# Optimization experiments

Measured on AMD Instinct MI355X. Metric: run time of the kernel, lower is better.

The kernel has to match this reference:

```python
import jax, jax.numpy as jnp
import numpy as np

DIM = 384
HEADS = 12
WS = (7, 7, 7)
N = WS[0] * WS[1] * WS[2]  # 343
NW = 64   # number of windows (mask dim)
B_ = 64   # num_windows * batch
CPB_HIDDEN = 512


def _make_buffers():
    # relative coords table: (1, 2Wd-1, 2Wh-1, 2Ww-1, 3), log-spaced per Swin-V2
    axes = [np.arange(-(w - 1), w, dtype=np.float32) / (w - 1) for w in WS]
    g = np.stack(np.meshgrid(*axes, indexing='ij'), axis=-1)[None]  # (1,13,13,13,3)
    g = g * 8.0
    table = np.sign(g) * np.log2(np.abs(g) + 1.0) / np.log2(8.0)
    # relative position index: (N, N) int
    coords = np.stack(np.meshgrid(*[np.arange(w) for w in WS], indexing='ij'))  # (3,Wd,Wh,Ww)
    cf = coords.reshape(3, -1)
    rel = (cf[:, :, None] - cf[:, None, :]).transpose(1, 2, 0).astype(np.int64)  # (N,N,3)
    rel[..., 0] += WS[0] - 1
    rel[..., 1] += WS[1] - 1
    rel[..., 2] += WS[2] - 1
    rel[..., 0] *= (2 * WS[1] - 1) * (2 * WS[2] - 1)
    rel[..., 1] *= 2 * WS[2] - 1
    idx = rel.sum(-1)
    return jnp.asarray(table, dtype=jnp.float32), jnp.asarray(idx, dtype=jnp.int32)


def setup_inputs() -> dict:
    key = jax.random.key(0)
    ks = jax.random.split(key, 10)
    table, idx = _make_buffers()
    return {
        'x': jax.random.normal(ks[0], (B_, N, DIM), dtype=jnp.float32),
        'mask': jax.random.normal(ks[1], (NW, N, N), dtype=jnp.float32),
        'qkv_w': jax.random.normal(ks[2], (3 * DIM, DIM), dtype=jnp.float32) * 0.02,
        'q_bias': jax.random.normal(ks[3], (DIM,), dtype=jnp.float32) * 0.02,
        'v_bias': jax.random.normal(ks[4], (DIM,), dtype=jnp.float32) * 0.02,
        'logit_scale': jnp.log(10.0 * jnp.ones((HEADS, 1, 1), dtype=jnp.float32)),
        'cpb_w1': jax.random.normal(ks[5], (CPB_HIDDEN, 3), dtype=jnp.float32) * 0.02,
        'cpb_b1': jax.random.normal(ks[6], (CPB_HIDDEN,), dtype=jnp.float32) * 0.02,
        'cpb_w2': jax.random.normal(ks[7], (HEADS, CPB_HIDDEN), dtype=jnp.float32) * 0.02,
        'proj_w': jax.random.normal(ks[8], (DIM, DIM), dtype=jnp.float32) * 0.02,
        'proj_b': jax.random.normal(ks[9], (DIM,), dtype=jnp.float32) * 0.02,
        'rel_table': table,
        'rel_index': idx,
    }


def reference(x, mask, qkv_w, q_bias, v_bias, logit_scale, cpb_w1, cpb_b1,
              cpb_w2, proj_w, proj_b, rel_table, rel_index):
    Bw, n, C = x.shape
    H = logit_scale.shape[0]
    hd = C // H
    qkv_bias = jnp.concatenate([q_bias, jnp.zeros_like(v_bias), v_bias])
    qkv = x @ qkv_w.T + qkv_bias                      # (Bw, n, 3C)
    qkv = qkv.reshape(Bw, n, 3, H, hd).transpose(2, 0, 3, 1, 4)
    q, k, v = qkv[0], qkv[1], qkv[2]                  # (Bw, H, n, hd)
    qn = q / jnp.clip(jnp.linalg.norm(q, axis=-1, keepdims=True), 1e-12)
    kn = k / jnp.clip(jnp.linalg.norm(k, axis=-1, keepdims=True), 1e-12)
    attn = jnp.einsum('bhnd,bhmd->bhnm', qn, kn)
    scale = jnp.exp(jnp.minimum(logit_scale, jnp.log(100.0)))  # clamp max log(1/0.01)
    attn = attn * scale
    # CPB MLP bias: (1,13,13,13,3) -> (table_size, H), gathered to (H, n, n)
    hidden = jax.nn.relu(rel_table @ cpb_w1.T + cpb_b1)
    bias_table = (hidden @ cpb_w2.T).reshape(-1, H)
    bias = bias_table[rel_index.reshape(-1)].reshape(n, n, H).transpose(2, 0, 1)
    bias = 16.0 * jax.nn.sigmoid(bias)
    attn = attn + bias[None]
    nW = mask.shape[0]
    attn = attn.reshape(Bw // nW, nW, H, n, n) + mask[None, :, None]
    attn = attn.reshape(Bw, H, n, n)
    attn = jax.nn.softmax(attn, axis=-1)
    out = jnp.einsum('bhnm,bhmd->bnhd', attn, v).reshape(Bw, n, C)
    out = out @ proj_w.T + proj_b
    return out
```

## Files before the change

### kernel.cpp

```cpp
#include <hip/hip_runtime.h>
#include <hip/hip_bf16.h>
#include <stdint.h>


typedef __attribute__((ext_vector_type(4))) float f32x4;
typedef __attribute__((ext_vector_type(8))) short short8;

#define DIM   384
#define HEADS 12
#define NTOK  343
#define NPAD  352
#define BW    64
#define MROWS (BW*NTOK)
#define MPAD  22016
#define NN    (NTOK*NTOK)
#define BPAD  352
#define LOG2E 1.44269504089f
#define SMAX  48.0f

__device__ __forceinline__ unsigned short f2bf(float f) {
  unsigned u = __float_as_uint(f);
  u += 0x7FFF + ((u >> 16) & 1);
  return (unsigned short)(u >> 16);
}

__device__ __forceinline__ unsigned pk2bf(float lo, float hi) {
  return (__float_as_uint(hi) & 0xFFFF0000u) | (__float_as_uint(lo) >> 16);
}

__device__ __forceinline__ void gload_lds16(const void* g, void* l) {
  __builtin_amdgcn_global_load_lds(
      (const __attribute__((address_space(1))) void*)g,
      (__attribute__((address_space(3))) void*)l, 16, 0, 0);
}

__global__ __launch_bounds__(256) void cvt_bf16(const float* __restrict__ in,
                                                unsigned short* __restrict__ out,
                                                long nvalid, long ntotal) {
  long i = ((long)blockIdx.x * 256 + threadIdx.x) * 8;
  if (i >= ntotal) return;
  short8 o;
  if (i < nvalid) {
    const float4* p = (const float4*)(in + i);
    float4 a = p[0], b = p[1];
    o[0] = (short)f2bf(a.x); o[1] = (short)f2bf(a.y);
    o[2] = (short)f2bf(a.z); o[3] = (short)f2bf(a.w);
    o[4] = (short)f2bf(b.x); o[5] = (short)f2bf(b.y);
    o[6] = (short)f2bf(b.z); o[7] = (short)f2bf(b.w);
  } else {
    o = (short8)0;
  }
  *(short8*)(out + i) = o;
}

__global__ __launch_bounds__(64) void cpb_tab(const float* __restrict__ tbl,
                                              const float* __restrict__ w1,
                                              const float* __restrict__ b1,
                                              const float* __restrict__ w2,
                                              float* __restrict__ btab) {
  const int r = blockIdx.x, lane = threadIdx.x;
  const float t0 = tbl[r*3], t1 = tbl[r*3+1], t2 = tbl[r*3+2];
  float acc[12];
#pragma unroll
  for (int hh = 0; hh < 12; ++hh) acc[hh] = 0.f;
  for (int u = 0; u < 8; ++u) {
    const int j = lane * 8 + u;
    const float hd = fmaxf(w1[j*3]*t0 + w1[j*3+1]*t1 + w1[j*3+2]*t2 + b1[j], 0.f);
#pragma unroll
    for (int hh = 0; hh < 12; ++hh) acc[hh] += hd * w2[hh*512 + j];
  }
#pragma unroll
  for (int hh = 0; hh < 12; ++hh) {
    float v = acc[hh];
    for (int msk = 1; msk < 64; msk <<= 1) v += __shfl_xor(v, msk);
    if (lane == 0) btab[r*12 + hh] = v;
  }
}

__global__ __launch_bounds__(256) void bias_gather(const float* __restrict__ btab,
                                                   const int* __restrict__ ridx,
                                                   float* __restrict__ bfull) {
  const int blk = blockIdx.x;
  const int hh = blk / NTOK, i = blk % NTOK;
  for (int j = threadIdx.x; j < BPAD; j += 256) {
    float o = -1e9f;
    if (j < NTOK) {
      const int idx = ridx[i*NTOK + j];
      const float v = btab[idx*12 + hh];
      o = LOG2E * 16.f / (1.f + __expf(-v)) - SMAX;
    }
    bfull[(size_t)blk*BPAD + j] = o;
  }
}

template<int MODE>
__global__ __launch_bounds__(256, 2) void gemm_k(
    const unsigned short* __restrict__ A, const unsigned short* __restrict__ B,
    unsigned short* __restrict__ o_qn, unsigned short* __restrict__ o_kn,
    unsigned short* __restrict__ o_vT,
    const float* __restrict__ q_bias, const float* __restrict__ v_bias,
    const float* __restrict__ lsc,
    float* __restrict__ o_out, const float* __restrict__ proj_b) {
  __shared__ alignas(16) uint8_t lds[32768];
  const int tid = threadIdx.x, wave = tid >> 6, lane = tid & 63;
  const int row0 = blockIdx.x * 128, col0 = blockIdx.y * 128;
  const int wm = wave & 1, wn = wave >> 1;
  const int l15 = lane & 15, lq = lane >> 4;
  f32x4 acc[4][4];
#pragma unroll
  for (int i = 0; i < 4; ++i)
#pragma unroll
    for (int j = 0; j < 4; ++j) acc[i][j] = (f32x4)0.f;

  const int stg_row = wave * 8 + (lane >> 3);
  const int srcblk = (lane & 7) ^ (lane >> 3);

  for (int kt = 0; kt < 6; ++kt) {
    const int k0 = kt * 64;
#pragma unroll
    for (int c = 0; c < 4; ++c) {
      const int row = c * 32 + stg_row;
      gload_lds16(A + (size_t)(row0 + row) * DIM + k0 + srcblk * 8,
                  lds + c * 4096 + wave * 1024);
      gload_lds16(B + (size_t)(col0 + row) * DIM + k0 + srcblk * 8,
                  lds + 16384 + c * 4096 + wave * 1024);
    }
    __syncthreads();
#pragma unroll
    for (int s = 0; s < 2; ++s) {
      short8 af[4], bfr[4];
#pragma unroll
      for (int i = 0; i < 4; ++i) {
        const int r = wm * 64 + i * 16 + l15;
        af[i] = *(const short8*)(lds + r * 128 + (((s * 4) | lq) ^ (r & 7)) * 16);
        const int cc = wn * 64 + i * 16 + l15;
        bfr[i] = *(const short8*)(lds + 16384 + cc * 128 + (((s * 4) | lq) ^ (cc & 7)) * 16);
      }
#pragma unroll
      for (int i = 0; i < 4; ++i)
#pragma unroll
        for (int j = 0; j < 4; ++j)
          acc[i][j] = __builtin_amdgcn_mfma_f32_16x16x32_bf16(af[i], bfr[j], acc[i][j], 0, 0, 0);
    }
    __syncthreads();
  }

  if (MODE == 0) {
#pragma unroll
    for (int i = 0; i < 4; ++i) {
      const int gr0 = row0 + wm * 64 + i * 16 + lq * 4;
#pragma unroll
      for (int p = 0; p < 2; ++p) {
        f32x4 c0 = acc[i][2 * p], c1 = acc[i][2 * p + 1];
        const int gcb = col0 + wn * 64 + p * 32;
        const int which = gcb / DIM, rem = gcb % DIM, hh = rem / 32;
        float b0 = 0.f, b1 = 0.f;
        if (which == 0) { b0 = q_bias[rem + l15]; b1 = q_bias[rem + l15 + 16]; }
        else if (which == 2) { b0 = v_bias[rem + l15]; b1 = v_bias[rem + l15 + 16]; }
#pragma unroll
        for (int r = 0; r < 4; ++r) { c0[r] += b0; c1[r] += b1; }
        float mult[4] = {1.f, 1.f, 1.f, 1.f};
        if (which < 2) {
          f32x4 ss;
#pragma unroll
          for (int r = 0; r < 4; ++r) ss[r] = c0[r] * c0[r] + c1[r] * c1[r];
#pragma unroll
          for (int msk = 1; msk < 16; msk <<= 1) {
#pragma unroll
            for (int r = 0; r < 4; ++r) ss[r] += __shfl_xor(ss[r], msk);
          }
          float sc = 1.f;
          if (which == 0)
            sc = __expf(fminf(lsc[hh], 4.6051701860f)) * LOG2E;
#pragma unroll
          for (int r = 0; r < 4; ++r) mult[r] = sc / fmaxf(sqrtf(ss[r]), 1e-12f);
        }
#pragma unroll
        for (int r = 0; r < 4; ++r) {
          const int gr = gr0 + r;
          if (gr >= MROWS) continue;
          const int b = gr / NTOK, nt = gr % NTOK;
          const unsigned short v0 = f2bf(c0[r] * mult[r]);
          const unsigned short v1 = f2bf(c1[r] * mult[r]);
          if (which == 0) {
            const size_t base = ((size_t)(b * HEADS + hh) * NTOK + nt) * 32 + l15;
            o_qn[base] = v0; o_qn[base + 16] = v1;
          } else if (which == 1) {
            const size_t base = ((size_t)(b * HEADS + hh) * NTOK + nt) * 32 + l15;
            o_kn[base] = v0; o_kn[base + 16] = v1;
          } else {
            const size_t base = ((size_t)(b * HEADS + hh) * 32 + l15) * NPAD + nt;
            o_vT[base] = v0; o_vT[base + (size_t)16 * NPAD] = v1;
          }
        }
      }
    }
  } else {
#pragma unroll
    for (int i = 0; i < 4; ++i) {
      const int gr0 = row0 + wm * 64 + i * 16 + lq * 4;
#pragma unroll
      for (int j = 0; j < 4; ++j) {
        const int gc = col0 + wn * 64 + j * 16 + l15;
        const float pb = proj_b[gc];
#pragma unroll
        for (int r = 0; r < 4; ++r) {
          const int gr = gr0 + r;
          if (gr < MROWS) o_out[(size_t)gr * DIM + gc] = acc[i][j][r] + pb;
        }
      }
    }
  }
}

__global__ __launch_bounds__(256, 3) void attn_k(
    const unsigned short* __restrict__ qn, const unsigned short* __restrict__ kn,
    const unsigned short* __restrict__ vT, const float* __restrict__ bfull,
    const float* __restrict__ mask, unsigned short* __restrict__ out1) {
  __shared__ alignas(16) uint8_t lds[38400];
  const int g = blockIdx.x;
  const int b = (g & 7) * 8 + (g >> 3) / HEADS;
  const int hh = (g >> 3) % HEADS;
  const int bh = b * HEADS + hh;
  const int tid = threadIdx.x;

  for (int r = tid; r < NPAD; r += 256) {
    uint4* dst = (uint4*)(lds + r * 80);
    if (r < NTOK) {
      const uint4* src = (const uint4*)(kn + ((size_t)bh * NTOK + r) * 32);
      dst[0] = src[0]; dst[1] = src[1]; dst[2] = src[2]; dst[3] = src[3];
    } else {
      uint4 z = make_uint4(0, 0, 0, 0);
      dst[0] = z; dst[1] = z; dst[2] = z; dst[3] = z;
    }
  }
  __syncthreads();

  const int wave = tid >> 6, lane = tid & 63;
  const int l15 = lane & 15, lq = lane >> 4;
  uint8_t* pb0 = lds + 28160 + wave * 2560;
  uint8_t* pb1 = pb0 + 1280;

  const unsigned short* vrow0 = vT + ((size_t)bh * 32 + 2 * l15) * NPAD;
  const unsigned short* vrow1 = vT + ((size_t)bh * 32 + 2 * l15 + 1) * NPAD;

  for (int t = wave; t < 22; t += 4) {
    const int q0 = t * 16;
    const int qc = min(q0 + l15, NTOK - 1);
    const short8 aq = *(const short8*)(qn + ((size_t)bh * NTOK + qc) * 32 + lq * 8);
    const float* brow = bfull + ((size_t)hh * NTOK + qc) * BPAD;
    const float* mrow = mask + (size_t)b * NN + (size_t)qc * NTOK;

    f32x4 o0 = (f32x4)0.f, o1 = (f32x4)0.f;
    float l_run = 0.f;

    f32x4 pbA[2], pbB[2];
    float pmA[2][4], pmB[2][4];
    short8 kf0[2], kf1[2], vf0[2], vf1[2];

    pbA[0] = *(const f32x4*)(brow + lq * 4);
    pbB[0] = *(const f32x4*)(brow + 16 + lq * 4);
    pbA[1] = *(const f32x4*)(brow + 32 + lq * 4);
    pbB[1] = *(const f32x4*)(brow + 48 + lq * 4);
#pragma unroll
    for (int r = 0; r < 4; ++r) {
      pmA[0][r] = mrow[lq * 4 + r];
      pmB[0][r] = mrow[16 + lq * 4 + r];
      pmA[1][r] = mrow[32 + lq * 4 + r];
      pmB[1][r] = mrow[48 + lq * 4 + r];
    }
    kf0[0] = *(const short8*)(lds + l15 * 80 + lq * 16);
    kf1[0] = *(const short8*)(lds + (16 + l15) * 80 + lq * 16);
    vf0[0] = *(const short8*)(vrow0 + lq * 8);
    vf1[0] = *(const short8*)(vrow1 + lq * 8);

#pragma unroll
    for (int c = 0; c <= 10; ++c) {
      const int cur = c & 1, nxt = cur ^ 1;
      const f32x4 cBA = pbA[cur], cBB = pbB[cur];
      float cMA[4], cMB[4];
#pragma unroll
      for (int r = 0; r < 4; ++r) { cMA[r] = pmA[cur][r]; cMB[r] = pmB[cur][r]; }
      const short8 vA = vf0[nxt], vB = vf1[nxt];
      if (c <= 8) {
        const int k2 = (c + 2) * 32;
        pbA[cur] = *(const f32x4*)(brow + k2 + lq * 4);
        pbB[cur] = *(const f32x4*)(brow + k2 + 16 + lq * 4);
#pragma unroll
        for (int r = 0; r < 4; ++r) {
          pmA[cur][r] = mrow[k2 + lq * 4 + r];
          const int kk = k2 + 16 + lq * 4 + r;
          pmB[cur][r] = mrow[(c == 8 && kk >= NTOK) ? 0 : kk];
        }
      }
      if (c <= 9) {
        const int k1 = (c + 1) * 32;
        vf0[nxt] = *(const short8*)(vrow0 + k1 + lq * 8);
        vf1[nxt] = *(const short8*)(vrow1 + k1 + lq * 8);
        kf0[nxt] = *(const short8*)(lds + (k1 + l15) * 80 + lq * 16);
        kf1[nxt] = *(const short8*)(lds + (k1 + 16 + l15) * 80 + lq * 16);
      }
      short8 pf;
      if (c > 0) pf = *(const short8*)((nxt ? pb1 : pb0) + l15 * 80 + lq * 16);
      f32x4 s0 = __builtin_amdgcn_mfma_f32_16x16x32_bf16(kf0[cur], aq, (f32x4)0.f, 0, 0, 0);
      f32x4 s1 = __builtin_amdgcn_mfma_f32_16x16x32_bf16(kf1[cur], aq, (f32x4)0.f, 0, 0, 0);
      float p0[4], p1[4], ps = 0.f;
#pragma unroll
      for (int r = 0; r < 4; ++r) {
        p0[r] = exp2f(s0[r] + fmaf(cMA[r], LOG2E, cBA[r]));
        p1[r] = exp2f(s1[r] + fmaf(cMB[r], LOG2E, cBB[r]));
        ps += p0[r] + p1[r];
      }
      l_run += ps;
      uint8_t* pw = (cur ? pb1 : pb0) + l15 * 80;
      *(uint2*)(pw + lq * 8)      = make_uint2(pk2bf(p0[0], p0[1]), pk2bf(p0[2], p0[3]));
      *(uint2*)(pw + 32 + lq * 8) = make_uint2(pk2bf(p1[0], p1[1]), pk2bf(p1[2], p1[3]));
      if (c > 0) {
        o0 = __builtin_amdgcn_mfma_f32_16x16x32_bf16(pf, vA, o0, 0, 0, 0);
        o1 = __builtin_amdgcn_mfma_f32_16x16x32_bf16(pf, vB, o1, 0, 0, 0);
      }
    }
    {
      const short8 pf = *(const short8*)(pb0 + l15 * 80 + lq * 16);
      o0 = __builtin_amdgcn_mfma_f32_16x16x32_bf16(pf, vf0[0], o0, 0, 0, 0);
      o1 = __builtin_amdgcn_mfma_f32_16x16x32_bf16(pf, vf1[0], o1, 0, 0, 0);
    }
    l_run += __shfl_xor(l_run, 16);
    l_run += __shfl_xor(l_run, 32);
    const float invl = 1.f / l_run;
    float ir[4];
#pragma unroll
    for (int r = 0; r < 4; ++r) ir[r] = __shfl(invl, lq * 4 + r);
#pragma unroll
    for (int r = 0; r < 4; ++r) {
      const int q = q0 + lq * 4 + r;
      if (q < NTOK) {
        const size_t base = ((size_t)b * NTOK + q) * DIM + hh * 32 + 2 * l15;
        *(unsigned*)(out1 + base) =
            (((unsigned)f2bf(o1[r] * ir[r])) << 16) | f2bf(o0[r] * ir[r]);
      }
    }
  }
}

extern "C" void kernel_launch(void* const* d_in, const int* in_sizes, int n_in,
                              void* d_out, int out_size, void* d_ws, size_t ws_size,
                              hipStream_t stream) {
  const float* x      = (const float*)d_in[0];
  const float* mask   = (const float*)d_in[1];
  const float* qkv_w  = (const float*)d_in[2];
  const float* q_bias = (const float*)d_in[3];
  const float* v_bias = (const float*)d_in[4];
  const float* lsc    = (const float*)d_in[5];
  const float* cpb_w1 = (const float*)d_in[6];
  const float* cpb_b1 = (const float*)d_in[7];
  const float* cpb_w2 = (const float*)d_in[8];
  const float* proj_w = (const float*)d_in[9];
  const float* proj_b = (const float*)d_in[10];
  const float* rtab   = (const float*)d_in[11];
  const int*   ridx   = (const int*)d_in[12];
  float* out = (float*)d_out;
  uint8_t* ws = (uint8_t*)d_ws;

  size_t o = 0;
  auto alloc = [&](size_t bytes) { size_t r = o; o += (bytes + 255) & ~(size_t)255; return r; };
  const size_t off_xb  = alloc((size_t)MPAD * DIM * 2);
  const size_t off_qwb = alloc((size_t)1152 * DIM * 2);
  const size_t off_pwb = alloc((size_t)DIM * DIM * 2);
  const size_t off_qnb = alloc((size_t)BW * HEADS * NTOK * 32 * 2);
  const size_t off_knb = alloc((size_t)BW * HEADS * NTOK * 32 * 2);
  const size_t off_vTb = alloc((size_t)BW * HEADS * 32 * NPAD * 2);
  const size_t off_btab  = alloc((size_t)2197 * 12 * 4);
  const size_t off_bfull = alloc((size_t)HEADS * NTOK * BPAD * 4);
  (void)in_sizes; (void)n_in; (void)out_size;

  if (ws_size < o) {
    hipMemsetAsync(d_out, 0, (size_t)out_size * 4, stream);
    return;
  }

  unsigned short* xb  = (unsigned short*)(ws + off_xb);
  unsigned short* o1b = xb;
  unsigned short* qwb = (unsigned short*)(ws + off_qwb);
  unsigned short* pwb = (unsigned short*)(ws + off_pwb);
  unsigned short* qnb = (unsigned short*)(ws + off_qnb);
  unsigned short* knb = (unsigned short*)(ws + off_knb);
  unsigned short* vTb = (unsigned short*)(ws + off_vTb);
  float* btab  = (float*)(ws + off_btab);
  float* bfull = (float*)(ws + off_bfull);

  cvt_bf16<<<(long)MPAD * DIM / 8 / 256, 256, 0, stream>>>(x, xb, (long)MROWS * DIM, (long)MPAD * DIM);
  cvt_bf16<<<1152 * DIM / 8 / 256, 256, 0, stream>>>(qkv_w, qwb, 1152L * DIM, 1152L * DIM);
  cvt_bf16<<<DIM * DIM / 8 / 256, 256, 0, stream>>>(proj_w, pwb, (long)DIM * DIM, (long)DIM * DIM);
  cpb_tab<<<2197, 64, 0, stream>>>(rtab, cpb_w1, cpb_b1, cpb_w2, btab);
  bias_gather<<<HEADS * NTOK, 256, 0, stream>>>(btab, ridx, bfull);
  gemm_k<0><<<dim3(MPAD / 128, 1152 / 128), 256, 0, stream>>>(
      xb, qwb, qnb, knb, vTb, q_bias, v_bias, lsc, nullptr, nullptr);
  attn_k<<<BW * HEADS, 256, 0, stream>>>(qnb, knb, vTb, bfull, mask, o1b);
  gemm_k<1><<<dim3(MPAD / 128, DIM / 128), 256, 0, stream>>>(
      o1b, pwb, nullptr, nullptr, nullptr, nullptr, nullptr, nullptr, out, proj_b);
}
```

Measured before the change: 322.8 us.

## Split attention into one-wave blocks per query tile and pre-pad scaled mask

The attention kernel now launches one 64-thread block per (window, head, 16-query tile) instead of one 256-thread block per (window, head) that staged all of K in LDS. K fragments are read straight from global memory, which drops the LDS fill and the block barrier and raises the block count for better occupancy and load balance. A new mask_pad kernel copies the mask into a 352-wide padded layout pre-multiplied by log2(e), so the attention loop can use vector loads without bounds checks and one fewer FMA. In exchange, K is re-read from global or L2 by each of the 22 query tiles, and the extra pass writes about 31 MB of padded mask and reads it back.

```diff
diff --git a/kernel.cpp b/kernel.cpp
--- a/kernel.cpp
+++ b/kernel.cpp
@@ -91,6 +91,15 @@
     }
     bfull[(size_t)blk*BPAD + j] = o;
   }
+}
+
+__global__ __launch_bounds__(128) void mask_pad(const float* __restrict__ mask,
+                                                float* __restrict__ maskp) {
+  const int row = blockIdx.x;
+  const float* src = mask + (size_t)row * NTOK;
+  float* dst = maskp + (size_t)row * BPAD;
+  for (int j = threadIdx.x; j < BPAD; j += 128)
+    dst[j] = (j < NTOK) ? src[j] * LOG2E : 0.f;
 }
 
 template<int MODE>
@@ -213,132 +222,110 @@
   }
 }
 
-__global__ __launch_bounds__(256, 3) void attn_k(
+__global__ __launch_bounds__(64) void attn_k(
     const unsigned short* __restrict__ qn, const unsigned short* __restrict__ kn,
     const unsigned short* __restrict__ vT, const float* __restrict__ bfull,
-    const float* __restrict__ mask, unsigned short* __restrict__ out1) {
-  __shared__ alignas(16) uint8_t lds[38400];
+    const float* __restrict__ maskp, unsigned short* __restrict__ out1) {
+  __shared__ alignas(16) uint8_t lds[2560];
   const int g = blockIdx.x;
-  const int b = (g & 7) * 8 + (g >> 3) / HEADS;
-  const int hh = (g >> 3) % HEADS;
+  const int hi = g >> 3;
+  const int b = (g & 7) * 8 + hi / 264;
+  const int rem = hi % 264;
+  const int hh = rem / 22, t = rem % 22;
   const int bh = b * HEADS + hh;
-  const int tid = threadIdx.x;
-
-  for (int r = tid; r < NPAD; r += 256) {
-    uint4* dst = (uint4*)(lds + r * 80);
-    if (r < NTOK) {
-      const uint4* src = (const uint4*)(kn + ((size_t)bh * NTOK + r) * 32);
-      dst[0] = src[0]; dst[1] = src[1]; dst[2] = src[2]; dst[3] = src[3];
-    } else {
-      uint4 z = make_uint4(0, 0, 0, 0);
-      dst[0] = z; dst[1] = z; dst[2] = z; dst[3] = z;
-    }
-  }
-  __syncthreads();
-
-  const int wave = tid >> 6, lane = tid & 63;
+  const int lane = threadIdx.x;
   const int l15 = lane & 15, lq = lane >> 4;
-  uint8_t* pb0 = lds + 28160 + wave * 2560;
-  uint8_t* pb1 = pb0 + 1280;
+  uint8_t* pb0 = lds;
+  uint8_t* pb1 = lds + 1280;
 
   const unsigned short* vrow0 = vT + ((size_t)bh * 32 + 2 * l15) * NPAD;
   const unsigned short* vrow1 = vT + ((size_t)bh * 32 + 2 * l15 + 1) * NPAD;
-
-  for (int t = wave; t < 22; t += 4) {
-    const int q0 = t * 16;
-    const int qc = min(q0 + l15, NTOK - 1);
-    const short8 aq = *(const short8*)(qn + ((size_t)bh * NTOK + qc) * 32 + lq * 8);
-    const float* brow = bfull + ((size_t)hh * NTOK + qc) * BPAD;
-    const float* mrow = mask + (size_t)b * NN + (size_t)qc * NTOK;
-
-    f32x4 o0 = (f32x4)0.f, o1 = (f32x4)0.f;
-    float l_run = 0.f;
-
-    f32x4 pbA[2], pbB[2];
-    float pmA[2][4], pmB[2][4];
-    short8 kf0[2], kf1[2], vf0[2], vf1[2];
-
-    pbA[0] = *(const f32x4*)(brow + lq * 4);
-    pbB[0] = *(const f32x4*)(brow + 16 + lq * 4);
-    pbA[1] = *(const f32x4*)(brow + 32 + lq * 4);
-    pbB[1] = *(const f32x4*)(brow + 48 + lq * 4);
+  const unsigned short* krow = kn + (size_t)bh * NTOK * 32;
+
+  const int q0 = t * 16;
+  const int qc = min(q0 + l15, NTOK - 1);
+  const short8 aq = *(const short8*)(qn + ((size_t)bh * NTOK + qc) * 32 + lq * 8);
+  const float* brow = bfull + ((size_t)hh * NTOK + qc) * BPAD;
+  const float* mrow = maskp + ((size_t)b * NTOK + qc) * BPAD;
+
+  f32x4 o0 = (f32x4)0.f, o1 = (f32x4)0.f;
+  float l_run = 0.f;
+
+  f32x4 pbA[2], pbB[2];
+  f32x4 pmA[2], pmB[2];
+  short8 kf0[2], kf1[2], vf0[2], vf1[2];
+
+  pbA[0] = *(const f32x4*)(brow + lq * 4);
+  pbB[0] = *(const f32x4*)(brow + 16 + lq * 4);
+  pbA[1] = *(const f32x4*)(brow + 32 + lq * 4);
+  pbB[1] = *(const f32x4*)(brow + 48 + lq * 4);
+  pmA[0] = *(const f32x4*)(mrow + lq * 4);
+  pmB[0] = *(const f32x4*)(mrow + 16 + lq * 4);
+  pmA[1] = *(const f32x4*)(mrow + 32 + lq * 4);
+  pmB[1] = *(const f32x4*)(mrow + 48 + lq * 4);
+  kf0[0] = *(const short8*)(krow + (size_t)l15 * 32 + lq * 8);
+  kf1[0] = *(const short8*)(krow + (size_t)(16 + l15) * 32 + lq * 8);
+  vf0[0] = *(const short8*)(vrow0 + lq * 8);
+  vf1[0] = *(const short8*)(vrow1 + lq * 8);
+
+#pragma unroll
+  for (int c = 0; c <= 10; ++c) {
+    const int cur = c & 1, nxt = cur ^ 1;
+    const f32x4 cBA = pbA[cur], cBB = pbB[cur];
+    const f32x4 cMA = pmA[cur], cMB = pmB[cur];
+    const short8 vA = vf0[nxt], vB = vf1[nxt];
+    if (c <= 8) {
+      const int k2 = (c + 2) * 32;
+      pbA[cur] = *(const f32x4*)(brow + k2 + lq * 4);
+      pbB[cur] = *(const f32x4*)(brow + k2 + 16 + lq * 4);
+      pmA[cur] = *(const f32x4*)(mrow + k2 + lq * 4);
+      pmB[cur] = *(const f32x4*)(mrow + k2 + 16 + lq * 4);
+    }
+    if (c <= 9) {
+      const int k1 = (c + 1) * 32;
+      vf0[nxt] = *(const short8*)(vrow0 + k1 + lq * 8);
+      vf1[nxt] = *(const short8*)(vrow1 + k1 + lq * 8);
+      kf0[nxt] = *(const short8*)(krow + (size_t)(k1 + l15) * 32 + lq * 8);
+      kf1[nxt] = *(const short8*)(krow + (size_t)(k1 + 16 + l15) * 32 + lq * 8);
+    }
+    short8 pf;
+    if (c > 0) pf = *(const short8*)((nxt ? pb1 : pb0) + l15 * 80 + lq * 16);
+    f32x4 s0 = __builtin_amdgcn_mfma_f32_16x16x32_bf16(kf0[cur], aq, (f32x4)0.f, 0, 0, 0);
+    f32x4 s1 = __builtin_amdgcn_mfma_f32_16x16x32_bf16(kf1[cur], aq, (f32x4)0.f, 0, 0, 0);
+    float p0[4], p1[4], ps = 0.f;
 #pragma unroll
     for (int r = 0; r < 4; ++r) {
-      pmA[0][r] = mrow[lq * 4 + r];
-      pmB[0][r] = mrow[16 + lq * 4 + r];
-      pmA[1][r] = mrow[32 + lq * 4 + r];
-      pmB[1][r] = mrow[48 + lq * 4 + r];
-    }
-    kf0[0] = *(const short8*)(lds + l15 * 80 + lq * 16);
-    kf1[0] = *(const short8*)(lds + (16 + l15) * 80 + lq * 16);
-    vf0[0] = *(const short8*)(vrow0 + lq * 8);
-    vf1[0] = *(const short8*)(vrow1 + lq * 8);
-
-#pragma unroll
-    for (int c = 0; c <= 10; ++c) {
-      const int cur = c & 1, nxt = cur ^ 1;
-      const f32x4 cBA = pbA[cur], cBB = pbB[cur];
-      float cMA[4], cMB[4];
-#pragma unroll
-      for (int r = 0; r < 4; ++r) { cMA[r] = pmA[cur][r]; cMB[r] = pmB[cur][r]; }
-      const short8 vA = vf0[nxt], vB = vf1[nxt];
-      if (c <= 8) {
-        const int k2 = (c + 2) * 32;
-        pbA[cur] = *(const f32x4*)(brow + k2 + lq * 4);
-        pbB[cur] = *(const f32x4*)(brow + k2 + 16 + lq * 4);
-#pragma unroll
-        for (int r = 0; r < 4; ++r) {
-          pmA[cur][r] = mrow[k2 + lq * 4 + r];
-          const int kk = k2 + 16 + lq * 4 + r;
-          pmB[cur][r] = mrow[(c == 8 && kk >= NTOK) ? 0 : kk];
-        }
-      }
-      if (c <= 9) {
-        const int k1 = (c + 1) * 32;
-        vf0[nxt] = *(const short8*)(vrow0 + k1 + lq * 8);
-        vf1[nxt] = *(const short8*)(vrow1 + k1 + lq * 8);
-        kf0[nxt] = *(const short8*)(lds + (k1 + l15) * 80 + lq * 16);
-        kf1[nxt] = *(const short8*)(lds + (k1 + 16 + l15) * 80 + lq * 16);
-      }
-      short8 pf;
-      if (c > 0) pf = *(const short8*)((nxt ? pb1 : pb0) + l15 * 80 + lq * 16);
-      f32x4 s0 = __builtin_amdgcn_mfma_f32_16x16x32_bf16(kf0[cur], aq, (f32x4)0.f, 0, 0, 0);
-      f32x4 s1 = __builtin_amdgcn_mfma_f32_16x16x32_bf16(kf1[cur], aq, (f32x4)0.f, 0, 0, 0);
-      float p0[4], p1[4], ps = 0.f;
-#pragma unroll
-      for (int r = 0; r < 4; ++r) {
-        p0[r] = exp2f(s0[r] + fmaf(cMA[r], LOG2E, cBA[r]));
-        p1[r] = exp2f(s1[r] + fmaf(cMB[r], LOG2E, cBB[r]));
-        ps += p0[r] + p1[r];
-      }
-      l_run += ps;
-      uint8_t* pw = (cur ? pb1 : pb0) + l15 * 80;
-      *(uint2*)(pw + lq * 8)      = make_uint2(pk2bf(p0[0], p0[1]), pk2bf(p0[2], p0[3]));
-      *(uint2*)(pw + 32 + lq * 8) = make_uint2(pk2bf(p1[0], p1[1]), pk2bf(p1[2], p1[3]));
-      if (c > 0) {
-        o0 = __builtin_amdgcn_mfma_f32_16x16x32_bf16(pf, vA, o0, 0, 0, 0);
-        o1 = __builtin_amdgcn_mfma_f32_16x16x32_bf16(pf, vB, o1, 0, 0, 0);
-      }
-    }
-    {
-      const short8 pf = *(const short8*)(pb0 + l15 * 80 + lq * 16);
-      o0 = __builtin_amdgcn_mfma_f32_16x16x32_bf16(pf, vf0[0], o0, 0, 0, 0);
-      o1 = __builtin_amdgcn_mfma_f32_16x16x32_bf16(pf, vf1[0], o1, 0, 0, 0);
-    }
-    l_run += __shfl_xor(l_run, 16);
-    l_run += __shfl_xor(l_run, 32);
-    const float invl = 1.f / l_run;
-    float ir[4];
-#pragma unroll
-    for (int r = 0; r < 4; ++r) ir[r] = __shfl(invl, lq * 4 + r);
-#pragma unroll
-    for (int r = 0; r < 4; ++r) {
-      const int q = q0 + lq * 4 + r;
-      if (q < NTOK) {
-        const size_t base = ((size_t)b * NTOK + q) * DIM + hh * 32 + 2 * l15;
-        *(unsigned*)(out1 + base) =
-            (((unsigned)f2bf(o1[r] * ir[r])) << 16) | f2bf(o0[r] * ir[r]);
-      }
+      p0[r] = exp2f(s0[r] + cBA[r] + cMA[r]);
+      p1[r] = exp2f(s1[r] + cBB[r] + cMB[r]);
+      ps += p0[r] + p1[r];
+    }
+    l_run += ps;
+    uint8_t* pw = (cur ? pb1 : pb0) + l15 * 80;
+    *(uint2*)(pw + lq * 8)      = make_uint2(pk2bf(p0[0], p0[1]), pk2bf(p0[2], p0[3]));
+    *(uint2*)(pw + 32 + lq * 8) = make_uint2(pk2bf(p1[0], p1[1]), pk2bf(p1[2], p1[3]));
+    if (c > 0) {
+      o0 = __builtin_amdgcn_mfma_f32_16x16x32_bf16(pf, vA, o0, 0, 0, 0);
+      o1 = __builtin_amdgcn_mfma_f32_16x16x32_bf16(pf, vB, o1, 0, 0, 0);
+    }
+  }
+  {
+    const short8 pf = *(const short8*)(pb0 + l15 * 80 + lq * 16);
+    o0 = __builtin_amdgcn_mfma_f32_16x16x32_bf16(pf, vf0[0], o0, 0, 0, 0);
+    o1 = __builtin_amdgcn_mfma_f32_16x16x32_bf16(pf, vf1[0], o1, 0, 0, 0);
+  }
+  l_run += __shfl_xor(l_run, 16);
+  l_run += __shfl_xor(l_run, 32);
+  const float invl = 1.f / l_run;
+  float ir[4];
+#pragma unroll
+  for (int r = 0; r < 4; ++r) ir[r] = __shfl(invl, lq * 4 + r);
+#pragma unroll
+  for (int r = 0; r < 4; ++r) {
+    const int q = q0 + lq * 4 + r;
+    if (q < NTOK) {
+      const size_t base = ((size_t)b * NTOK + q) * DIM + hh * 32 + 2 * l15;
+      *(unsigned*)(out1 + base) =
+          (((unsigned)f2bf(o1[r] * ir[r])) << 16) | f2bf(o0[r] * ir[r]);
     }
   }
 }
@@ -372,6 +359,7 @@
   const size_t off_vTb = alloc((size_t)BW * HEADS * 32 * NPAD * 2);
   const size_t off_btab  = alloc((size_t)2197 * 12 * 4);
   const size_t off_bfull = alloc((size_t)HEADS * NTOK * BPAD * 4);
+  const size_t off_maskp = alloc((size_t)BW * NTOK * BPAD * 4);
   (void)in_sizes; (void)n_in; (void)out_size;
 
   if (ws_size < o) {
@@ -388,15 +376,17 @@
   unsigned short* vTb = (unsigned short*)(ws + off_vTb);
   float* btab  = (float*)(ws + off_btab);
   float* bfull = (float*)(ws + off_bfull);
+  float* maskp = (float*)(ws + off_maskp);
 
   cvt_bf16<<<(long)MPAD * DIM / 8 / 256, 256, 0, stream>>>(x, xb, (long)MROWS * DIM, (long)MPAD * DIM);
   cvt_bf16<<<1152 * DIM / 8 / 256, 256, 0, stream>>>(qkv_w, qwb, 1152L * DIM, 1152L * DIM);
   cvt_bf16<<<DIM * DIM / 8 / 256, 256, 0, stream>>>(proj_w, pwb, (long)DIM * DIM, (long)DIM * DIM);
   cpb_tab<<<2197, 64, 0, stream>>>(rtab, cpb_w1, cpb_b1, cpb_w2, btab);
   bias_gather<<<HEADS * NTOK, 256, 0, stream>>>(btab, ridx, bfull);
+  mask_pad<<<BW * NTOK, 128, 0, stream>>>(mask, maskp);
   gemm_k<0><<<dim3(MPAD / 128, 1152 / 128), 256, 0, stream>>>(
       xb, qwb, qnb, knb, vTb, q_bias, v_bias, lsc, nullptr, nullptr);
-  attn_k<<<BW * HEADS, 256, 0, stream>>>(qnb, knb, vTb, bfull, mask, o1b);
+  attn_k<<<8 * 8 * HEADS * 22, 64, 0, stream>>>(qnb, knb, vTb, bfull, maskp, o1b);
   gemm_k<1><<<dim3(MPAD / 128, DIM / 128), 256, 0, stream>>>(
       o1b, pwb, nullptr, nullptr, nullptr, nullptr, nullptr, nullptr, out, proj_b);
 }
```

New measurement: 378.9 us. 17.4% more time.
